# Kernel tuning notes

Hardware: AMD Instinct MI355X
Metric: run time of the kernel (lower is better)

## Reference

```python
import jax, jax.numpy as jnp
import numpy as np

# Flattened-state gather indices. State is prev[9,3] flattened to 27 values,
# then concat with x -> flat[29], where flat[27]=a=x[0], flat[28]=b=x[1].
# Row t gives the (x0, x1, x2) inputs of triangle t, read from the source wiring.
IDX0 = np.array([3, 0, 6, 12, 9, 15, 18, 6, 15])   # x0 inputs
IDX1 = np.array([1, 7, 4, 19, 16, 13, 10, 22, 25])  # x1 inputs
IDX2 = np.array([17, 5, 11, 8, 28, 2, 27, 23, 26])  # x2 inputs (t=4 -> b, t=6 -> a)

NOISE_SCALE = 0.125  # LUT2 hard-codes noise = 0.125


def mux(s, a, b):
    return 0.5 * (s * b - s * a + a + b)


def setup_inputs() -> dict:
    key = jax.random.key(0)
    k1, k2, k3 = jax.random.split(key, 3)
    x = jax.random.normal(k1, (2,), dtype=jnp.float32)
    weights = jax.random.normal(k2, (9, 3, 4), dtype=jnp.float32)  # 9 triangles x 3 LUT2s x 4 weights
    noise = jax.random.normal(k3, (130, 9, 3, 4), dtype=jnp.float32)  # per-step np.random.normal draws
    return {"x": x, "weights": weights, "noise": noise, "dummy1": 0, "dummy2": 0}


def reference(x, weights, noise, dummy1, dummy2):
    del dummy1, dummy2  # unused in the original forward

    def step(prev, n):
        # prev: [9,3] current states; n: [9,3,4] noise for this step
        flat = jnp.concatenate([prev.reshape(-1), x])  # [29]
        x0, x1, x2 = flat[IDX0], flat[IDX1], flat[IDX2]  # each [9]
        # LUT j of each triangle: LUT0(x1,x2), LUT1(x0,x2), LUT2(x0,x1)
        A = jnp.stack([x1, x0, x0], axis=1)  # [9,3] first mux select
        B = jnp.stack([x2, x2, x1], axis=1)  # [9,3] second mux select
        w = weights + jnp.abs(1.0 - jnp.abs(weights)) * n * NOISE_SCALE  # [9,3,4]
        m0 = mux(A, w[..., 0], w[..., 1])
        m1 = mux(A, w[..., 2], w[..., 3])
        new = mux(B, m0, m1)  # [9,3] synchronous update (uupdate after all forwards)
        return new, None

    init = -jnp.ones((9, 3), dtype=x.dtype)  # all states start at -1
    final, _ = jax.lax.scan(step, init, noise)  # 130 steps
    return jnp.stack([final[0, 1], final[1, 2], final[7, 2]])
```

## Files before the change

kernel.cpp:

```cpp
#include <hip/hip_runtime.h>


#define STEPS 130
#define NLUT  27
#define ROUNDS 65

__device__ __constant__ int c_idx0[9] = {3, 0, 6, 12, 9, 15, 18, 6, 15};
__device__ __constant__ int c_idx1[9] = {1, 7, 4, 19, 16, 13, 10, 22, 25};
__device__ __constant__ int c_idx2[9] = {17, 5, 11, 8, 28, 2, 27, 23, 26};

__device__ __forceinline__ int wA(int m) {
    int t = m / 3, j = m % 3;
    return (j == 0) ? c_idx1[t] : c_idx0[t];
}
__device__ __forceinline__ int wB(int m) {
    int t = m / 3, j = m % 3;
    int s = (j == 2) ? c_idx1[t] : c_idx2[t];
    return (s >= NLUT) ? 0 : s;
}

__device__ __forceinline__ float evalE(float4 k, float x, float y) {
    return fmaf(y, fmaf(x, k.x, k.y), fmaf(x, k.z, k.w));
}

__device__ __forceinline__ float bperm(int byteIdx, float v) {
    return __int_as_float(__builtin_amdgcn_ds_bpermute(byteIdx, __float_as_int(v)));
}

__global__ __launch_bounds__(1024)
void one_layer_net_kernel(const float* __restrict__ x,
                          const float* __restrict__ weights,
                          const float* __restrict__ noise,
                          float* __restrict__ out) {
    __shared__ float4 tbl[STEPS * NLUT];

    const int tid = threadIdx.x;
    const float a = x[0];
    const float b = x[1];

    const float4* __restrict__ w4 = (const float4*)weights;
    const float4* __restrict__ n4 = (const float4*)noise;
    for (int i = tid; i < STEPS * NLUT; i += 1024) {
        const int l = i % NLUT;
        float4 w = w4[l];
        float4 n = n4[i];
        float w0 = fmaf(fabsf(1.0f - fabsf(w.x)) * n.x, 0.125f, w.x);
        float w1 = fmaf(fabsf(1.0f - fabsf(w.y)) * n.y, 0.125f, w.y);
        float w2 = fmaf(fabsf(1.0f - fabsf(w.z)) * n.z, 0.125f, w.z);
        float w3 = fmaf(fabsf(1.0f - fabsf(w.w)) * n.w, 0.125f, w.w);
        float d0 = w1 - w0, s0 = w0 + w1;
        float d1 = w3 - w2, s1 = w2 + w3;
        float K3 = 0.25f * (d1 - d0);
        float K2 = 0.25f * (s1 - s0);
        float K1 = 0.25f * (d0 + d1);
        float K0 = 0.25f * (s0 + s1);
        if (l == 12 || l == 13) {
            K0 = fmaf(K2, b, K0); K1 = fmaf(K3, b, K1); K2 = 0.0f; K3 = 0.0f;
        }
        if (l == 18 || l == 19) {
            K0 = fmaf(K2, a, K0); K1 = fmaf(K3, a, K1); K2 = 0.0f; K3 = 0.0f;
        }
        tbl[i] = make_float4(K3, K2, K1, K0);
    }
    __syncthreads();

    if (tid >= 64) return;

    const int l  = tid;
    const int lc = (l < NLUT) ? l : (NLUT - 1);

    const int a0 = wA(lc), b0 = wB(lc);
    const int g0 = wA(a0) << 2, g1 = wB(a0) << 2;
    const int g2 = wA(b0) << 2, g3 = wB(b0) << 2;

    const float4* __restrict__ pA = tbl + 0 * NLUT + a0;
    const float4* __restrict__ pB = tbl + 0 * NLUT + b0;
    const float4* __restrict__ pC = tbl + 1 * NLUT + lc;

    float state = -1.0f;

    #pragma unroll
    for (int r = 0; r < ROUNDS; ++r) {
        const int o = r * 2 * NLUT;
        const float q0 = bperm(g0, state);
        const float q1 = bperm(g1, state);
        const float q2 = bperm(g2, state);
        const float q3 = bperm(g3, state);
        const float4 kA = pA[o];
        const float4 kB = pB[o];
        const float4 kC = pC[o];
        const float u1 = evalE(kA, q0, q1);
        const float u2 = evalE(kB, q2, q3);
        state = evalE(kC, u1, u2);
    }

    if (l == 1)  out[0] = state;
    if (l == 5)  out[1] = state;
    if (l == 23) out[2] = state;
}

extern "C" void kernel_launch(void* const* d_in, const int* in_sizes, int n_in,
                              void* d_out, int out_size, void* d_ws, size_t ws_size,
                              hipStream_t stream) {
    const float* x       = (const float*)d_in[0];
    const float* weights = (const float*)d_in[1];
    const float* noise   = (const float*)d_in[2];
    float* out = (float*)d_out;
    one_layer_net_kernel<<<1, 1024, 0, stream>>>(x, weights, noise, out);
}
```

Before: 64.89 us.

## Stage coefficient table in global workspace and prefetch rounds into registers

Coefficient table moves from LDS to the global workspace buffer. The serial recurrence loop now prefetches table entries six rounds ahead into register ring buffers, so LDS reads no longer sit on the critical path next to the bpermute chain. The block size drops from 1024 to 512 threads. This adds global-memory write/read latency and relies on __threadfence_block plus syncthreads for visibility within a single block.

```diff
diff --git a/kernel.cpp b/kernel.cpp
--- a/kernel.cpp
+++ b/kernel.cpp
@@ -4,6 +4,7 @@
 #define STEPS 130
 #define NLUT  27
 #define ROUNDS 65
+#define PF     6
 
 __device__ __constant__ int c_idx0[9] = {3, 0, 6, 12, 9, 15, 18, 6, 15};
 __device__ __constant__ int c_idx1[9] = {1, 7, 4, 19, 16, 13, 10, 22, 25};
@@ -27,20 +28,19 @@
     return __int_as_float(__builtin_amdgcn_ds_bpermute(byteIdx, __float_as_int(v)));
 }
 
-__global__ __launch_bounds__(1024)
+__global__ __launch_bounds__(512)
 void one_layer_net_kernel(const float* __restrict__ x,
                           const float* __restrict__ weights,
                           const float* __restrict__ noise,
-                          float* __restrict__ out) {
-    __shared__ float4 tbl[STEPS * NLUT];
-
+                          float* __restrict__ out,
+                          float4* __restrict__ gK) {
     const int tid = threadIdx.x;
     const float a = x[0];
     const float b = x[1];
 
     const float4* __restrict__ w4 = (const float4*)weights;
     const float4* __restrict__ n4 = (const float4*)noise;
-    for (int i = tid; i < STEPS * NLUT; i += 1024) {
+    for (int i = tid; i < STEPS * NLUT; i += 512) {
         const int l = i % NLUT;
         float4 w = w4[l];
         float4 n = n4[i];
@@ -60,8 +60,9 @@
         if (l == 18 || l == 19) {
             K0 = fmaf(K2, a, K0); K1 = fmaf(K3, a, K1); K2 = 0.0f; K3 = 0.0f;
         }
-        tbl[i] = make_float4(K3, K2, K1, K0);
+        gK[i] = make_float4(K3, K2, K1, K0);
     }
+    __threadfence_block();
     __syncthreads();
 
     if (tid >= 64) return;
@@ -73,25 +74,35 @@
     const int g0 = wA(a0) << 2, g1 = wB(a0) << 2;
     const int g2 = wA(b0) << 2, g3 = wB(b0) << 2;
 
-    const float4* __restrict__ pA = tbl + 0 * NLUT + a0;
-    const float4* __restrict__ pB = tbl + 0 * NLUT + b0;
-    const float4* __restrict__ pC = tbl + 1 * NLUT + lc;
+    const float4* __restrict__ pA = gK + 0 * NLUT + a0;
+    const float4* __restrict__ pB = gK + 0 * NLUT + b0;
+    const float4* __restrict__ pC = gK + 1 * NLUT + lc;
+
+    float4 bufA[PF], bufB[PF], bufC[PF];
+    #pragma unroll
+    for (int r = 0; r < PF; ++r) {
+        const int o = r * 2 * NLUT;
+        bufA[r] = pA[o]; bufB[r] = pB[o]; bufC[r] = pC[o];
+    }
 
     float state = -1.0f;
 
     #pragma unroll
     for (int r = 0; r < ROUNDS; ++r) {
-        const int o = r * 2 * NLUT;
         const float q0 = bperm(g0, state);
         const float q1 = bperm(g1, state);
         const float q2 = bperm(g2, state);
         const float q3 = bperm(g3, state);
-        const float4 kA = pA[o];
-        const float4 kB = pB[o];
-        const float4 kC = pC[o];
+        const float4 kA = bufA[r % PF];
+        const float4 kB = bufB[r % PF];
+        const float4 kC = bufC[r % PF];
         const float u1 = evalE(kA, q0, q1);
         const float u2 = evalE(kB, q2, q3);
         state = evalE(kC, u1, u2);
+        if (r + PF < ROUNDS) {
+            const int o = (r + PF) * 2 * NLUT;
+            bufA[r % PF] = pA[o]; bufB[r % PF] = pB[o]; bufC[r % PF] = pC[o];
+        }
     }
 
     if (l == 1)  out[0] = state;
@@ -105,6 +116,7 @@
     const float* x       = (const float*)d_in[0];
     const float* weights = (const float*)d_in[1];
     const float* noise   = (const float*)d_in[2];
-    float* out = (float*)d_out;
-    one_layer_net_kernel<<<1, 1024, 0, stream>>>(x, weights, noise, out);
+    float* out  = (float*)d_out;
+    float4* gK  = (float4*)d_ws;
+    one_layer_net_kernel<<<1, 512, 0, stream>>>(x, weights, noise, out, gK);
 }
```

After: 70.36 us. 8.4% more time.
